# Performance work log

Measured on AMD Instinct MI355X. Metric: run time of the kernel, lower is better.

## Reference

```python
import jax, jax.numpy as jnp
import numpy as np

B, S, H, NH = 1, 4096, 768, 12
D = H // NH  # per-head dim = 64


def setup_inputs() -> dict:
    key = jax.random.key(0)
    ks = jax.random.split(key, 10)
    p = 0.02  # param scale
    return {
        "x": jax.random.normal(ks[0], (B, S, H), jnp.float32),
        "Wq": jax.random.normal(ks[1], (H, H), jnp.float32) * p,
        "bq": jax.random.normal(ks[2], (H,), jnp.float32) * p,
        "Wk": jax.random.normal(ks[3], (H, H), jnp.float32) * p,
        "bk": jax.random.normal(ks[4], (H,), jnp.float32) * p,
        "Wv": jax.random.normal(ks[5], (H, H), jnp.float32) * p,
        "bv": jax.random.normal(ks[6], (H,), jnp.float32) * p,
        "Wo": jax.random.normal(ks[7], (H, H), jnp.float32) * p,
        "bo": jax.random.normal(ks[8], (H,), jnp.float32) * p,
        "attn_mask": jax.random.randint(ks[9], (B, 1, 1, S), 0, 2).astype(bool),
    }


def _split_heads(t):
    # [B, S, H] -> [B, NH, S, D]
    return t.reshape(B, S, NH, D).transpose(0, 2, 1, 3)


def reference(x, Wq, bq, Wk, bk, Wv, bv, Wo, bo, attn_mask):
    q = _split_heads(x @ Wq.T + bq)
    k = _split_heads(x @ Wk.T + bk)
    v = _split_heads(x @ Wv.T + bv)
    scores = jnp.einsum('bhqd,bhkd->bhqk', q, k) / np.sqrt(D).astype(np.float32)
    scores = jnp.where(attn_mask, jnp.float32(-1e9), scores)
    attn = jax.nn.softmax(scores, axis=-1)
    ctx = jnp.einsum('bhqk,bhkd->bhqd', attn, v)
    ctx = ctx.transpose(0, 2, 1, 3).reshape(B, S, H)  # merge heads
    return ctx @ Wo.T + bo
```

## Files before the change

kernel.cpp:

```cpp
#include <hip/hip_runtime.h>
#include <stdint.h>

#define S_LEN 4096
#define HDIM  768
#define NHEAD 12
#define DHEAD 64

typedef _Float16 f16;
typedef __attribute__((ext_vector_type(8)))  _Float16 f16x8;
typedef __attribute__((ext_vector_type(4)))  _Float16 f16x4;
typedef __attribute__((ext_vector_type(4)))  float    f32x4;
typedef __attribute__((ext_vector_type(16))) float    f32x16;

typedef __attribute__((address_space(1))) void gv_t;
typedef __attribute__((address_space(3))) void lv_t;

__device__ __forceinline__ void async_copy16(const void* g, void* l) {
  __builtin_amdgcn_global_load_lds((gv_t*)g, (lv_t*)l, 16, 0, 0);
}

__device__ __forceinline__ float fast_exp2(float x) {
#if __has_builtin(__builtin_amdgcn_exp2f)
  return __builtin_amdgcn_exp2f(x);
#else
  return exp2f(x);
#endif
}

__device__ __forceinline__ int swz4(int row) { return (row ^ (row >> 2)) & 3; }

constexpr size_t OFF_META = 0;
constexpr size_t OFF_POS  = 256;
constexpr size_t OFF_XB   = 65536;
constexpr size_t SZ_XB    = (size_t)S_LEN * HDIM * 2;
constexpr size_t OFF_WQKV = OFF_XB + SZ_XB;
constexpr size_t SZ_WQKV  = (size_t)3 * HDIM * HDIM * 2;
constexpr size_t OFF_WO   = OFF_WQKV + SZ_WQKV;
constexpr size_t SZ_WO    = (size_t)HDIM * HDIM * 2;
constexpr size_t OFF_Q    = OFF_WO + SZ_WO;
constexpr size_t SZ_HD    = (size_t)NHEAD * S_LEN * DHEAD * 2;
constexpr size_t OFF_K    = OFF_Q + SZ_HD;
constexpr size_t OFF_VT   = OFF_K + SZ_HD;
constexpr size_t OFF_VR   = OFF_VT + SZ_HD;
constexpr size_t OFF_PO1  = OFF_VR + SZ_HD;

__global__ __launch_bounds__(256) void k_prep(const float* __restrict__ x,
                                              const float* __restrict__ wq,
                                              const float* __restrict__ wk,
                                              const float* __restrict__ wv,
                                              const float* __restrict__ wo,
                                              const int* __restrict__ mi,
                                              f16* __restrict__ dst,
                                              f16* __restrict__ Kc,
                                              int* __restrict__ pos,
                                              int* __restrict__ meta) {
  __shared__ int s_flag;
  __shared__ int s_cnt[256];
  const int b = blockIdx.x, tid = threadIdx.x;
  if (b < 5376) {
    int i = b * 256 + tid;
    const float* src; int off;
    if (i < 786432) { src = x; off = i; }
    else {
      int j = i - 786432;
      int w = j / 147456;
      off = j - w * 147456;
      src = (w == 0) ? wq : (w == 1) ? wk : (w == 2) ? wv : wo;
    }
    float4 v = ((const float4*)src)[off];
    f16x4 h;
    h[0] = (f16)v.x; h[1] = (f16)v.y; h[2] = (f16)v.z; h[3] = (f16)v.w;
    ((f16x4*)dst)[i] = h;
    return;
  }
  if (b < 6144) {
    int u = (b - 5376) * 512 + tid;
    f16x8 z = {};
    ((f16x8*)Kc)[u] = z;
    ((f16x8*)Kc)[u + 256] = z;
    return;
  }
  if (tid == 0) s_flag = 1;
  __syncthreads();
  int bad = 0;
  #pragma unroll
  for (int k = 0; k < 4; ++k) {
    int v = mi[k * 256 + tid];
    if (v != 0 && v != 1) bad = 1;
  }
  if (bad) atomicAnd(&s_flag, 0);
  __syncthreads();
  const int isInt = s_flag;
  const unsigned char* mu8 = (const unsigned char*)mi;
  int keep[16]; int cnt = 0;
  const int s0 = tid * 16;
  #pragma unroll
  for (int k = 0; k < 16; ++k) {
    int mval = isInt ? mi[s0 + k] : (int)mu8[s0 + k];
    keep[k] = (mval == 0) ? 1 : 0;
    cnt += keep[k];
  }
  s_cnt[tid] = cnt;
  __syncthreads();
  for (int off = 1; off < 256; off <<= 1) {
    int t = (tid >= off) ? s_cnt[tid - off] : 0;
    __syncthreads();
    s_cnt[tid] += t;
    __syncthreads();
  }
  int base = s_cnt[tid] - cnt;
  #pragma unroll
  for (int k = 0; k < 16; ++k) {
    pos[s0 + k] = keep[k] ? base : -1;
    base += keep[k];
  }
  if (tid == 255) meta[0] = s_cnt[255];
}

__global__ __launch_bounds__(256) void k_qkv(
    const f16* __restrict__ xb, const f16* __restrict__ wqkv,
    const float* __restrict__ bq, const float* __restrict__ bk, const float* __restrict__ bv,
    const int* __restrict__ pos,
    f16* __restrict__ Qh, f16* __restrict__ Kc, f16* __restrict__ Vrow) {
  __shared__ __attribute__((aligned(16))) f16 lA[128 * 32];
  __shared__ __attribute__((aligned(16))) f16 lB[128 * 32];
  const int tid = threadIdx.x;
  const int wid = tid >> 6, lane = tid & 63;
  const int quad = lane >> 4, l16 = lane & 15;
  const int wm = wid >> 1, wn = wid & 1;
  const int tn = blockIdx.x;
  const int m0 = blockIdx.y * 128;
  const int mat = tn / 6;
  const int nb = (tn % 6) * 128;
  const f16* wbase = wqkv + (size_t)mat * HDIM * HDIM;

  f32x4 acc[4][4] = {};

  for (int k0 = 0; k0 < HDIM; k0 += 32) {
    #pragma unroll
    for (int iss = 0; iss < 2; ++iss) {
      int c = iss * 256 + tid;
      int row = c >> 2, slot = c & 3;
      int gs = slot ^ swz4(row);
      async_copy16((const char*)(xb + (size_t)(m0 + row) * HDIM + k0) + gs * 16,
                   (char*)lA + (iss * 256 + wid * 64) * 16);
      async_copy16((const char*)(wbase + (size_t)(nb + row) * HDIM + k0) + gs * 16,
                   (char*)lB + (iss * 256 + wid * 64) * 16);
    }
    __syncthreads();
    f16x8 af[4], bf[4];
    #pragma unroll
    for (int mi = 0; mi < 4; ++mi) {
      int row = wm * 64 + mi * 16 + l16;
      af[mi] = *(const f16x8*)&lA[row * 32 + (quad ^ swz4(row)) * 8];
    }
    #pragma unroll
    for (int ni = 0; ni < 4; ++ni) {
      int row = wn * 64 + ni * 16 + l16;
      bf[ni] = *(const f16x8*)&lB[row * 32 + (quad ^ swz4(row)) * 8];
    }
    #pragma unroll
    for (int mi = 0; mi < 4; ++mi)
      #pragma unroll
      for (int ni = 0; ni < 4; ++ni)
        acc[mi][ni] = __builtin_amdgcn_mfma_f32_16x16x32_f16(af[mi], bf[ni], acc[mi][ni], 0, 0, 0);
    __syncthreads();
  }

  const float* bias = (mat == 0) ? bq : (mat == 1) ? bk : bv;
  const float qscale = 0.125f * 1.44269504088896341f;
  f16* kvdst = (mat == 1) ? Kc : Vrow;
  #pragma unroll
  for (int mi = 0; mi < 4; ++mi) {
    int srow = m0 + wm * 64 + mi * 16 + quad * 4;
    #pragma unroll
    for (int ni = 0; ni < 4; ++ni) {
      int n = nb + wn * 64 + ni * 16 + l16;
      int head = n >> 6, d = n & 63;
      float b = bias[n];
      #pragma unroll
      for (int r = 0; r < 4; ++r) {
        int s = srow + r;
        float val = acc[mi][ni][r] + b;
        if (mat == 0) {
          Qh[((size_t)head * S_LEN + s) * DHEAD + d] = (f16)(val * qscale);
        } else {
          int p = pos[s];
          if (p >= 0)
            kvdst[((size_t)head * S_LEN + p) * DHEAD + d] = (f16)val;
        }
      }
    }
  }
}

__global__ __launch_bounds__(256) void k_vt(const int* __restrict__ meta,
                                            const f16* __restrict__ Vrow,
                                            f16* __restrict__ Vtc) {
  const int kc = meta[0];
  const int kcp = (kc + 63) & ~63;
  const int p0 = blockIdx.x * 64;
  const int h = blockIdx.y;
  if (p0 >= kcp) return;
  __shared__ __attribute__((aligned(16))) f16 lT[64 * 80];
  const int tid = threadIdx.x;
  for (int u = tid; u < 512; u += 256) {
    int d8 = u >> 6, p = u & 63;
    f16x8 v = {};
    if (p0 + p < kc) v = *(const f16x8*)&Vrow[((size_t)h * S_LEN + p0 + p) * DHEAD + d8 * 8];
    #pragma unroll
    for (int j = 0; j < 8; ++j) lT[(d8 * 8 + j) * 80 + p] = v[j];
  }
  __syncthreads();
  for (int w = tid; w < 512; w += 256) {
    int d = w >> 3, p8 = w & 7;
    f16x8 o = *(const f16x8*)&lT[d * 80 + p8 * 8];
    *(f16x8*)&Vtc[((size_t)h * DHEAD + d) * S_LEN + p0 + p8 * 8] = o;
  }
}

__global__ __launch_bounds__(256) void k_attn(
    const f16* __restrict__ Qh, const f16* __restrict__ Kc, const f16* __restrict__ Vtc,
    const int* __restrict__ meta, f16* __restrict__ PO0, f16* __restrict__ PO1,
    float* __restrict__ PL) {
  __shared__ __attribute__((aligned(16))) f16 lK[64 * 64];
  __shared__ __attribute__((aligned(16))) f16 lV[64 * 64];
  __shared__ __attribute__((aligned(16))) f16 lP[4][32 * 64];
  const int tid = threadIdx.x;
  const int wid = tid >> 6, lane = tid & 63;
  const int hf = lane >> 5, q = lane & 31, r7 = q & 7;
  const int head = blockIdx.y;
  const int q0 = blockIdx.x * 128 + wid * 32;
  const int split = blockIdx.z;
  const int kc = meta[0];
  const int nkt = (kc + 63) >> 6;
  const int th = nkt >> 1;
  const int t0 = split ? th : 0;
  const int t1 = split ? nkt : th;
  const float npadf = split ? (float)(nkt * 64 - kc) : 0.f;

  const f16* Qp = Qh + ((size_t)head * S_LEN + q0 + q) * DHEAD;
  f16x8 qf[4];
  #pragma unroll
  for (int t = 0; t < 4; ++t) qf[t] = *(const f16x8*)(Qp + t * 16 + hf * 8);

  f32x16 accO0 = {}, accO1 = {};
  float lsum = 0.f;

  const char* kbase = (const char*)(Kc + (size_t)head * S_LEN * DHEAD);
  const char* vbase = (const char*)(Vtc + (size_t)head * DHEAD * S_LEN);
  f16* pw = &lP[wid][0];

  for (int it = t0; it < t1; ++it) {
    const int j0 = it * 64;
    #pragma unroll
    for (int iss = 0; iss < 2; ++iss) {
      int c = iss * 256 + tid;
      int row = c >> 3, slot = c & 7;
      int gs = slot ^ (row & 7);
      async_copy16(kbase + (size_t)(j0 + row) * 128 + gs * 16,
                   (char*)lK + (iss * 256 + wid * 64) * 16);
      async_copy16(vbase + (size_t)row * (S_LEN * 2) + (size_t)j0 * 2 + gs * 16,
                   (char*)lV + (iss * 256 + wid * 64) * 16);
    }
    __syncthreads();

    f32x16 sA = {}, sB = {};
    #pragma unroll
    for (int t = 0; t < 4; ++t) {
      int so = ((2 * t + hf) ^ r7) * 8;
      f16x8 a0 = *(const f16x8*)&lK[q * 64 + so];
      f16x8 a1 = *(const f16x8*)&lK[(32 + q) * 64 + so];
      sA = __builtin_amdgcn_mfma_f32_32x32x16_f16(a0, qf[t], sA, 0, 0, 0);
      sB = __builtin_amdgcn_mfma_f32_32x32x16_f16(a1, qf[t], sB, 0, 0, 0);
    }

    #pragma unroll
    for (int i = 0; i < 16; ++i) { sA[i] = fast_exp2(sA[i]); lsum += sA[i]; }
    #pragma unroll
    for (int i = 0; i < 16; ++i) { sB[i] = fast_exp2(sB[i]); lsum += sB[i]; }

    #pragma unroll
    for (int g = 0; g < 4; ++g) {
      f16x4 w0, w1;
      #pragma unroll
      for (int r = 0; r < 4; ++r) { w0[r] = (f16)sA[4 * g + r]; w1[r] = (f16)sB[4 * g + r]; }
      *(f16x4*)&pw[q * 64 + (g ^ r7) * 8 + hf * 4]       = w0;
      *(f16x4*)&pw[q * 64 + ((4 + g) ^ r7) * 8 + hf * 4] = w1;
    }

    #pragma unroll
    for (int t = 0; t < 4; ++t) {
      int so = ((2 * t + hf) ^ r7) * 8;
      f16x8 pf = *(const f16x8*)&pw[q * 64 + so];
      f16x8 v0 = *(const f16x8*)&lV[q * 64 + so];
      f16x8 v1 = *(const f16x8*)&lV[(32 + q) * 64 + so];
      accO0 = __builtin_amdgcn_mfma_f32_32x32x16_f16(pf, v0, accO0, 0, 0, 0);
      accO1 = __builtin_amdgcn_mfma_f32_32x32x16_f16(pf, v1, accO1, 0, 0, 0);
    }
    __syncthreads();
  }

  lsum += __shfl_xor(lsum, 32, 64);
  lsum -= npadf;
  if (hf == 0)
    PL[((size_t)split * NHEAD + head) * S_LEN + q0 + q] = lsum;

  f16* PO = split ? PO1 : PO0;
  #pragma unroll
  for (int reg = 0; reg < 16; ++reg) {
    int s = q0 + (reg & 3) + 8 * (reg >> 2) + 4 * hf;
    PO[((size_t)head * S_LEN + s) * DHEAD + q]      = (f16)accO0[reg];
    PO[((size_t)head * S_LEN + s) * DHEAD + 32 + q] = (f16)accO1[reg];
  }
}

__global__ __launch_bounds__(256) void k_comb(const f16* __restrict__ PO0,
                                              const f16* __restrict__ PO1,
                                              const float* __restrict__ PL,
                                              f16* __restrict__ ctx) {
  int u = blockIdx.x * 256 + threadIdx.x;
  int s = u / 96;
  int c = u - s * 96;
  int h = c >> 3, db = (c & 7) * 8;
  size_t i0 = ((size_t)h * S_LEN + s) * DHEAD + db;
  f16x8 o0 = *(const f16x8*)(PO0 + i0);
  f16x8 o1 = *(const f16x8*)(PO1 + i0);
  float l = PL[(size_t)h * S_LEN + s] + PL[(size_t)(NHEAD + h) * S_LEN + s];
  float inv = 1.0f / l;
  f16x8 o;
  #pragma unroll
  for (int i = 0; i < 8; ++i) o[i] = (f16)(((float)o0[i] + (float)o1[i]) * inv);
  *(f16x8*)(ctx + (size_t)s * HDIM + h * DHEAD + db) = o;
}

__global__ __launch_bounds__(256) void k_out(
    const f16* __restrict__ ctx, const f16* __restrict__ wo,
    const float* __restrict__ bo, float* __restrict__ out) {
  __shared__ __attribute__((aligned(16))) f16 lA[128 * 32];
  __shared__ __attribute__((aligned(16))) f16 lB[128 * 32];
  const int tid = threadIdx.x;
  const int wid = tid >> 6, lane = tid & 63;
  const int quad = lane >> 4, l16 = lane & 15;
  const int wm = wid >> 1, wn = wid & 1;
  const int nb = blockIdx.x * 128;
  const int m0 = blockIdx.y * 128;

  f32x4 acc[4][4] = {};

  for (int k0 = 0; k0 < HDIM; k0 += 32) {
    #pragma unroll
    for (int iss = 0; iss < 2; ++iss) {
      int c = iss * 256 + tid;
      int row = c >> 2, slot = c & 3;
      int gs = slot ^ swz4(row);
      async_copy16((const char*)(ctx + (size_t)(m0 + row) * HDIM + k0) + gs * 16,
                   (char*)lA + (iss * 256 + wid * 64) * 16);
      async_copy16((const char*)(wo + (size_t)(nb + row) * HDIM + k0) + gs * 16,
                   (char*)lB + (iss * 256 + wid * 64) * 16);
    }
    __syncthreads();
    f16x8 af[4], bf[4];
    #pragma unroll
    for (int mi = 0; mi < 4; ++mi) {
      int row = wm * 64 + mi * 16 + l16;
      af[mi] = *(const f16x8*)&lA[row * 32 + (quad ^ swz4(row)) * 8];
    }
    #pragma unroll
    for (int ni = 0; ni < 4; ++ni) {
      int row = wn * 64 + ni * 16 + l16;
      bf[ni] = *(const f16x8*)&lB[row * 32 + (quad ^ swz4(row)) * 8];
    }
    #pragma unroll
    for (int mi = 0; mi < 4; ++mi)
      #pragma unroll
      for (int ni = 0; ni < 4; ++ni)
        acc[mi][ni] = __builtin_amdgcn_mfma_f32_16x16x32_f16(af[mi], bf[ni], acc[mi][ni], 0, 0, 0);
    __syncthreads();
  }

  #pragma unroll
  for (int mi = 0; mi < 4; ++mi) {
    int srow = m0 + wm * 64 + mi * 16 + quad * 4;
    #pragma unroll
    for (int ni = 0; ni < 4; ++ni) {
      int n = nb + wn * 64 + ni * 16 + l16;
      float b = bo[n];
      #pragma unroll
      for (int r = 0; r < 4; ++r)
        out[(size_t)(srow + r) * HDIM + n] = acc[mi][ni][r] + b;
    }
  }
}

extern "C" void kernel_launch(void* const* d_in, const int* in_sizes, int n_in,
                              void* d_out, int out_size, void* d_ws, size_t ws_size,
                              hipStream_t stream) {
  const float* x  = (const float*)d_in[0];
  const float* Wq = (const float*)d_in[1];
  const float* bq = (const float*)d_in[2];
  const float* Wk = (const float*)d_in[3];
  const float* bk = (const float*)d_in[4];
  const float* Wv = (const float*)d_in[5];
  const float* bv = (const float*)d_in[6];
  const float* Wo = (const float*)d_in[7];
  const float* bo = (const float*)d_in[8];
  const int*   mask = (const int*)d_in[9];
  float* out = (float*)d_out;

  char* ws = (char*)d_ws;
  int* meta  = (int*)(ws + OFF_META);
  int* pos   = (int*)(ws + OFF_POS);
  f16* xb    = (f16*)(ws + OFF_XB);
  f16* wqkv  = (f16*)(ws + OFF_WQKV);
  f16* wob   = (f16*)(ws + OFF_WO);
  f16* Qh    = (f16*)(ws + OFF_Q);
  f16* Kc    = (f16*)(ws + OFF_K);
  f16* Vtc   = (f16*)(ws + OFF_VT);
  f16* Vrow  = (f16*)(ws + OFF_VR);
  f16* PO0   = (f16*)(ws + OFF_VR);
  f16* PO1   = (f16*)(ws + OFF_PO1);
  float* PL  = (float*)(ws + OFF_WQKV);
  f16* ctx   = (f16*)(ws + OFF_XB);

  k_prep<<<dim3(6145), 256, 0, stream>>>(x, Wq, Wk, Wv, Wo, mask, xb, Kc, pos, meta);
  k_qkv<<<dim3(18, 32), 256, 0, stream>>>(xb, wqkv, bq, bk, bv, pos, Qh, Kc, Vrow);
  k_vt<<<dim3(64, NHEAD), 256, 0, stream>>>(meta, Vrow, Vtc);
  k_attn<<<dim3(32, NHEAD, 2), 256, 0, stream>>>(Qh, Kc, Vtc, meta, PO0, PO1, PL);
  k_comb<<<dim3((S_LEN * 96) / 256), 256, 0, stream>>>(PO0, PO1, PL, ctx);
  k_out<<<dim3(6, 32), 256, 0, stream>>>(ctx, wob, bo, out);
}
```

Baseline: 192.4 us.

## Restructure attention kernel: 64-query warps, in-register P, intra-block key split

Each wavefront now handles 64 queries instead of 32, and the four warps split into two query groups times two key-tile streams. Each key stream owns its own K/V LDS buffer, loaded by separate warps. The exp'd scores are fed straight from registers into the PV MFMA, which removes the per-warp P round trip through LDS. The two key-stream partial outputs are merged through LDS at the end, and launch bounds request 3 blocks per CU. The V transpose store also now reads its LDS tile in 4-element pieces. The aim is more K/V reuse per LDS load and fewer LDS writes, at the cost of more accumulator registers and a final reduction step.

```diff
diff --git a/kernel.cpp b/kernel.cpp
--- a/kernel.cpp
+++ b/kernel.cpp
@@ -214,104 +214,154 @@
   __syncthreads();
   for (int w = tid; w < 512; w += 256) {
     int d = w >> 3, p8 = w & 7;
-    f16x8 o = *(const f16x8*)&lT[d * 80 + p8 * 8];
+    int base16 = (p8 >> 1) * 16, half = p8 & 1;
+    f16x4 lo = *(const f16x4*)&lT[d * 80 + base16 + half * 4];
+    f16x4 hi = *(const f16x4*)&lT[d * 80 + base16 + 8 + half * 4];
+    f16x8 o;
+    o[0] = lo[0]; o[1] = lo[1]; o[2] = lo[2]; o[3] = lo[3];
+    o[4] = hi[0]; o[5] = hi[1]; o[6] = hi[2]; o[7] = hi[3];
     *(f16x8*)&Vtc[((size_t)h * DHEAD + d) * S_LEN + p0 + p8 * 8] = o;
   }
 }
 
-__global__ __launch_bounds__(256) void k_attn(
+__global__ __launch_bounds__(256, 3) void k_attn(
     const f16* __restrict__ Qh, const f16* __restrict__ Kc, const f16* __restrict__ Vtc,
     const int* __restrict__ meta, f16* __restrict__ PO0, f16* __restrict__ PO1,
     float* __restrict__ PL) {
-  __shared__ __attribute__((aligned(16))) f16 lK[64 * 64];
-  __shared__ __attribute__((aligned(16))) f16 lV[64 * 64];
-  __shared__ __attribute__((aligned(16))) f16 lP[4][32 * 64];
+  __shared__ __attribute__((aligned(16))) f16 lbuf[2][2][64 * 64];
+  __shared__ float lcomb[2][64];
   const int tid = threadIdx.x;
   const int wid = tid >> 6, lane = tid & 63;
-  const int hf = lane >> 5, q = lane & 31, r7 = q & 7;
+  const int hf = lane >> 5, l31 = lane & 31;
+  const int qg = wid & 1, ks = wid >> 1;
   const int head = blockIdx.y;
-  const int q0 = blockIdx.x * 128 + wid * 32;
   const int split = blockIdx.z;
+  const int qbase = blockIdx.x * 128 + qg * 64;
   const int kc = meta[0];
   const int nkt = (kc + 63) >> 6;
   const int th = nkt >> 1;
   const int t0 = split ? th : 0;
   const int t1 = split ? nkt : th;
-  const float npadf = split ? (float)(nkt * 64 - kc) : 0.f;
-
-  const f16* Qp = Qh + ((size_t)head * S_LEN + q0 + q) * DHEAD;
-  f16x8 qf[4];
-  #pragma unroll
-  for (int t = 0; t < 4; ++t) qf[t] = *(const f16x8*)(Qp + t * 16 + hf * 8);
-
-  f32x16 accO0 = {}, accO1 = {};
-  float lsum = 0.f;
+  const int nloop = (t1 - t0 + 1) >> 1;
+
+  f16x8 qf[2][4];
+  #pragma unroll
+  for (int qh = 0; qh < 2; ++qh) {
+    const f16* Qp = Qh + ((size_t)head * S_LEN + qbase + qh * 32 + l31) * DHEAD;
+    #pragma unroll
+    for (int dc = 0; dc < 4; ++dc)
+      qf[qh][dc] = *(const f16x8*)(Qp + dc * 16 + hf * 8);
+  }
+
+  f32x16 accO[2][2] = {};
+  float lsum[2] = {0.f, 0.f};
 
   const char* kbase = (const char*)(Kc + (size_t)head * S_LEN * DHEAD);
   const char* vbase = (const char*)(Vtc + (size_t)head * DHEAD * S_LEN);
-  f16* pw = &lP[wid][0];
-
-  for (int it = t0; it < t1; ++it) {
-    const int j0 = it * 64;
-    #pragma unroll
-    for (int iss = 0; iss < 2; ++iss) {
-      int c = iss * 256 + tid;
-      int row = c >> 3, slot = c & 7;
-      int gs = slot ^ (row & 7);
-      async_copy16(kbase + (size_t)(j0 + row) * 128 + gs * 16,
-                   (char*)lK + (iss * 256 + wid * 64) * 16);
-      async_copy16(vbase + (size_t)row * (S_LEN * 2) + (size_t)j0 * 2 + gs * 16,
-                   (char*)lV + (iss * 256 + wid * 64) * 16);
-    }
-    __syncthreads();
-
-    f32x16 sA = {}, sB = {};
-    #pragma unroll
-    for (int t = 0; t < 4; ++t) {
-      int so = ((2 * t + hf) ^ r7) * 8;
-      f16x8 a0 = *(const f16x8*)&lK[q * 64 + so];
-      f16x8 a1 = *(const f16x8*)&lK[(32 + q) * 64 + so];
-      sA = __builtin_amdgcn_mfma_f32_32x32x16_f16(a0, qf[t], sA, 0, 0, 0);
-      sB = __builtin_amdgcn_mfma_f32_32x32x16_f16(a1, qf[t], sB, 0, 0, 0);
-    }
-
-    #pragma unroll
-    for (int i = 0; i < 16; ++i) { sA[i] = fast_exp2(sA[i]); lsum += sA[i]; }
-    #pragma unroll
-    for (int i = 0; i < 16; ++i) { sB[i] = fast_exp2(sB[i]); lsum += sB[i]; }
-
-    #pragma unroll
-    for (int g = 0; g < 4; ++g) {
-      f16x4 w0, w1;
-      #pragma unroll
-      for (int r = 0; r < 4; ++r) { w0[r] = (f16)sA[4 * g + r]; w1[r] = (f16)sB[4 * g + r]; }
-      *(f16x4*)&pw[q * 64 + (g ^ r7) * 8 + hf * 4]       = w0;
-      *(f16x4*)&pw[q * 64 + ((4 + g) ^ r7) * 8 + hf * 4] = w1;
-    }
-
-    #pragma unroll
-    for (int t = 0; t < 4; ++t) {
-      int so = ((2 * t + hf) ^ r7) * 8;
-      f16x8 pf = *(const f16x8*)&pw[q * 64 + so];
-      f16x8 v0 = *(const f16x8*)&lV[q * 64 + so];
-      f16x8 v1 = *(const f16x8*)&lV[(32 + q) * 64 + so];
-      accO0 = __builtin_amdgcn_mfma_f32_32x32x16_f16(pf, v0, accO0, 0, 0, 0);
-      accO1 = __builtin_amdgcn_mfma_f32_32x32x16_f16(pf, v1, accO1, 0, 0, 0);
-    }
-    __syncthreads();
-  }
-
-  lsum += __shfl_xor(lsum, 32, 64);
-  lsum -= npadf;
-  if (hf == 0)
-    PL[((size_t)split * NHEAD + head) * S_LEN + q0 + q] = lsum;
-
-  f16* PO = split ? PO1 : PO0;
-  #pragma unroll
-  for (int reg = 0; reg < 16; ++reg) {
-    int s = q0 + (reg & 3) + 8 * (reg >> 2) + 4 * hf;
-    PO[((size_t)head * S_LEN + s) * DHEAD + q]      = (f16)accO0[reg];
-    PO[((size_t)head * S_LEN + s) * DHEAD + 32 + q] = (f16)accO1[reg];
+  f16* myK = &lbuf[ks][0][0];
+  f16* myV = &lbuf[ks][1][0];
+  const int srow = lane >> 3, sslot = lane & 7;
+
+  for (int i = 0; i < nloop; ++i) {
+    const int t = t0 + 2 * i + ks;
+    const bool active = t < t1;
+    if (active) {
+      const int j0 = t * 64;
+      if (qg == 0) {
+        #pragma unroll
+        for (int r = 0; r < 8; ++r) {
+          int row = r * 8 + srow;
+          int gs = sslot ^ (row & 7);
+          async_copy16(kbase + (size_t)(j0 + row) * 128 + gs * 16, (char*)myK + r * 1024);
+        }
+      } else {
+        #pragma unroll
+        for (int r = 0; r < 8; ++r) {
+          int d = r * 8 + srow;
+          int gs = sslot ^ (d & 7);
+          async_copy16(vbase + (size_t)d * (S_LEN * 2) + (size_t)j0 * 2 + gs * 16,
+                       (char*)myV + r * 1024);
+        }
+      }
+    }
+    __syncthreads();
+    if (active) {
+      #pragma unroll
+      for (int mh = 0; mh < 2; ++mh) {
+        f16x8 af[4];
+        const int arow = mh * 32 + l31;
+        #pragma unroll
+        for (int dc = 0; dc < 4; ++dc) {
+          int c = dc * 2 + hf;
+          af[dc] = *(const f16x8*)&myK[arow * 64 + ((c ^ (arow & 7)) * 8)];
+        }
+        #pragma unroll
+        for (int qh = 0; qh < 2; ++qh) {
+          f32x16 s = {};
+          #pragma unroll
+          for (int dc = 0; dc < 4; ++dc)
+            s = __builtin_amdgcn_mfma_f32_32x32x16_f16(af[dc], qf[qh][dc], s, 0, 0, 0);
+          float ls = 0.f;
+          #pragma unroll
+          for (int u = 0; u < 16; ++u) { s[u] = fast_exp2(s[u]); ls += s[u]; }
+          lsum[qh] += ls;
+          #pragma unroll
+          for (int cc = 0; cc < 2; ++cc) {
+            f16x8 pf;
+            #pragma unroll
+            for (int u = 0; u < 8; ++u) pf[u] = (f16)s[8 * cc + u];
+            const int kt = mh * 2 + cc;
+            #pragma unroll
+            for (int dh = 0; dh < 2; ++dh) {
+              int vrow = dh * 32 + l31;
+              int c = kt * 2 + hf;
+              f16x8 vf = *(const f16x8*)&myV[vrow * 64 + ((c ^ (vrow & 7)) * 8)];
+              accO[qh][dh] = __builtin_amdgcn_mfma_f32_32x32x16_f16(pf, vf, accO[qh][dh], 0, 0, 0);
+            }
+          }
+        }
+      }
+    }
+    __syncthreads();
+  }
+
+  lsum[0] += __shfl_xor(lsum[0], 32);
+  lsum[1] += __shfl_xor(lsum[1], 32);
+  const float npadf = (float)(nkt * 64 - kc);
+  if (split == 1 && (((nkt - 1 - t0) & 1) == ks)) { lsum[0] -= npadf; lsum[1] -= npadf; }
+
+  float* ocomb = (float*)&lbuf[0][0][0];
+  if (ks == 1) {
+    #pragma unroll
+    for (int qh = 0; qh < 2; ++qh) {
+      #pragma unroll
+      for (int dh = 0; dh < 2; ++dh)
+        #pragma unroll
+        for (int reg = 0; reg < 16; ++reg) {
+          int row = qh * 32 + (reg & 3) + 8 * (reg >> 2) + 4 * hf;
+          ocomb[qg * 4096 + row * 64 + dh * 32 + l31] = accO[qh][dh][reg];
+        }
+      if (hf == 0) lcomb[qg][qh * 32 + l31] = lsum[qh];
+    }
+  }
+  __syncthreads();
+  if (ks == 0) {
+    f16* PO = split ? PO1 : PO0;
+    #pragma unroll
+    for (int qh = 0; qh < 2; ++qh) {
+      #pragma unroll
+      for (int dh = 0; dh < 2; ++dh)
+        #pragma unroll
+        for (int reg = 0; reg < 16; ++reg) {
+          int row = qh * 32 + (reg & 3) + 8 * (reg >> 2) + 4 * hf;
+          float v = accO[qh][dh][reg] + ocomb[qg * 4096 + row * 64 + dh * 32 + l31];
+          int sidx = qbase + row;
+          PO[((size_t)head * S_LEN + sidx) * DHEAD + dh * 32 + l31] = (f16)v;
+        }
+      if (hf == 0)
+        PL[((size_t)split * NHEAD + head) * S_LEN + qbase + qh * 32 + l31] =
+            lsum[qh] + lcomb[qg][qh * 32 + l31];
+    }
   }
 }
 
```

Measured after the change: 256.2 us. +33.2%, slower.

## Keep softmax probabilities in registers by permuting V columns to match MFMA layout

Applied to the files above, without the earlier changes.

The attention kernel no longer writes exp(scores) to per-wave LDS and reads them back as the A operand. Each 32-key score tile is converted to f16 in registers and fed straight into the PV MFMA. To keep that correct, the V transpose kernel interleaves groups of four keys so that V's key order matches the accumulator's register layout. The change also drops the lP shared buffer and adds an occupancy hint of 3 blocks per CU. It saves LDS traffic and capacity in the inner loop, at the cost of a tighter coupling between the V storage order and the MFMA output layout.

```diff
diff --git a/kernel.cpp b/kernel.cpp
--- a/kernel.cpp
+++ b/kernel.cpp
@@ -214,45 +214,47 @@
   __syncthreads();
   for (int w = tid; w < 512; w += 256) {
     int d = w >> 3, p8 = w & 7;
-    f16x8 o = *(const f16x8*)&lT[d * 80 + p8 * 8];
+    int base16 = (p8 >> 1) * 16, half = p8 & 1;
+    f16x4 lo = *(const f16x4*)&lT[d * 80 + base16 + half * 4];
+    f16x4 hi = *(const f16x4*)&lT[d * 80 + base16 + 8 + half * 4];
+    f16x8 o;
+    o[0] = lo[0]; o[1] = lo[1]; o[2] = lo[2]; o[3] = lo[3];
+    o[4] = hi[0]; o[5] = hi[1]; o[6] = hi[2]; o[7] = hi[3];
     *(f16x8*)&Vtc[((size_t)h * DHEAD + d) * S_LEN + p0 + p8 * 8] = o;
   }
 }
 
-__global__ __launch_bounds__(256) void k_attn(
+__global__ __launch_bounds__(256, 3) void k_attn(
     const f16* __restrict__ Qh, const f16* __restrict__ Kc, const f16* __restrict__ Vtc,
     const int* __restrict__ meta, f16* __restrict__ PO0, f16* __restrict__ PO1,
     float* __restrict__ PL) {
   __shared__ __attribute__((aligned(16))) f16 lK[64 * 64];
   __shared__ __attribute__((aligned(16))) f16 lV[64 * 64];
-  __shared__ __attribute__((aligned(16))) f16 lP[4][32 * 64];
   const int tid = threadIdx.x;
   const int wid = tid >> 6, lane = tid & 63;
-  const int hf = lane >> 5, q = lane & 31, r7 = q & 7;
+  const int hf = lane >> 5, l31 = lane & 31, r7 = l31 & 7;
   const int head = blockIdx.y;
+  const int split = blockIdx.z;
   const int q0 = blockIdx.x * 128 + wid * 32;
-  const int split = blockIdx.z;
   const int kc = meta[0];
   const int nkt = (kc + 63) >> 6;
   const int th = nkt >> 1;
   const int t0 = split ? th : 0;
   const int t1 = split ? nkt : th;
-  const float npadf = split ? (float)(nkt * 64 - kc) : 0.f;
-
-  const f16* Qp = Qh + ((size_t)head * S_LEN + q0 + q) * DHEAD;
+
+  const f16* Qp = Qh + ((size_t)head * S_LEN + q0 + l31) * DHEAD;
   f16x8 qf[4];
   #pragma unroll
-  for (int t = 0; t < 4; ++t) qf[t] = *(const f16x8*)(Qp + t * 16 + hf * 8);
-
-  f32x16 accO0 = {}, accO1 = {};
+  for (int dc = 0; dc < 4; ++dc) qf[dc] = *(const f16x8*)(Qp + dc * 16 + hf * 8);
+
+  f32x16 accO[2] = {};
   float lsum = 0.f;
 
   const char* kbase = (const char*)(Kc + (size_t)head * S_LEN * DHEAD);
   const char* vbase = (const char*)(Vtc + (size_t)head * DHEAD * S_LEN);
-  f16* pw = &lP[wid][0];
-
-  for (int it = t0; it < t1; ++it) {
-    const int j0 = it * 64;
+
+  for (int t = t0; t < t1; ++t) {
+    const int j0 = t * 64;
     #pragma unroll
     for (int iss = 0; iss < 2; ++iss) {
       int c = iss * 256 + tid;
@@ -265,54 +267,49 @@
     }
     __syncthreads();
 
-    f32x16 sA = {}, sB = {};
-    #pragma unroll
-    for (int t = 0; t < 4; ++t) {
-      int so = ((2 * t + hf) ^ r7) * 8;
-      f16x8 a0 = *(const f16x8*)&lK[q * 64 + so];
-      f16x8 a1 = *(const f16x8*)&lK[(32 + q) * 64 + so];
-      sA = __builtin_amdgcn_mfma_f32_32x32x16_f16(a0, qf[t], sA, 0, 0, 0);
-      sB = __builtin_amdgcn_mfma_f32_32x32x16_f16(a1, qf[t], sB, 0, 0, 0);
-    }
-
-    #pragma unroll
-    for (int i = 0; i < 16; ++i) { sA[i] = fast_exp2(sA[i]); lsum += sA[i]; }
-    #pragma unroll
-    for (int i = 0; i < 16; ++i) { sB[i] = fast_exp2(sB[i]); lsum += sB[i]; }
-
-    #pragma unroll
-    for (int g = 0; g < 4; ++g) {
-      f16x4 w0, w1;
-      #pragma unroll
-      for (int r = 0; r < 4; ++r) { w0[r] = (f16)sA[4 * g + r]; w1[r] = (f16)sB[4 * g + r]; }
-      *(f16x4*)&pw[q * 64 + (g ^ r7) * 8 + hf * 4]       = w0;
-      *(f16x4*)&pw[q * 64 + ((4 + g) ^ r7) * 8 + hf * 4] = w1;
-    }
-
-    #pragma unroll
-    for (int t = 0; t < 4; ++t) {
-      int so = ((2 * t + hf) ^ r7) * 8;
-      f16x8 pf = *(const f16x8*)&pw[q * 64 + so];
-      f16x8 v0 = *(const f16x8*)&lV[q * 64 + so];
-      f16x8 v1 = *(const f16x8*)&lV[(32 + q) * 64 + so];
-      accO0 = __builtin_amdgcn_mfma_f32_32x32x16_f16(pf, v0, accO0, 0, 0, 0);
-      accO1 = __builtin_amdgcn_mfma_f32_32x32x16_f16(pf, v1, accO1, 0, 0, 0);
-    }
-    __syncthreads();
-  }
-
-  lsum += __shfl_xor(lsum, 32, 64);
-  lsum -= npadf;
+    #pragma unroll
+    for (int mh = 0; mh < 2; ++mh) {
+      f16x8 af[4];
+      const int arow = mh * 32 + l31;
+      #pragma unroll
+      for (int dc = 0; dc < 4; ++dc)
+        af[dc] = *(const f16x8*)&lK[arow * 64 + ((((dc << 1) | hf) ^ r7) * 8)];
+      f32x16 s = {};
+      #pragma unroll
+      for (int dc = 0; dc < 4; ++dc)
+        s = __builtin_amdgcn_mfma_f32_32x32x16_f16(af[dc], qf[dc], s, 0, 0, 0);
+      #pragma unroll
+      for (int u = 0; u < 16; ++u) { s[u] = fast_exp2(s[u]); lsum += s[u]; }
+      #pragma unroll
+      for (int cc = 0; cc < 2; ++cc) {
+        f16x8 pf;
+        #pragma unroll
+        for (int u = 0; u < 8; ++u) pf[u] = (f16)s[8 * cc + u];
+        const int c2 = mh * 2 + cc;
+        #pragma unroll
+        for (int dh = 0; dh < 2; ++dh) {
+          const int vrow = dh * 32 + l31;
+          f16x8 vf = *(const f16x8*)&lV[vrow * 64 + ((((c2 << 1) | hf) ^ r7) * 8)];
+          accO[dh] = __builtin_amdgcn_mfma_f32_32x32x16_f16(pf, vf, accO[dh], 0, 0, 0);
+        }
+      }
+    }
+    __syncthreads();
+  }
+
+  lsum += __shfl_xor(lsum, 32);
+  if (split == 1) lsum -= (float)(nkt * 64 - kc);
   if (hf == 0)
-    PL[((size_t)split * NHEAD + head) * S_LEN + q0 + q] = lsum;
+    PL[((size_t)split * NHEAD + head) * S_LEN + q0 + l31] = lsum;
 
   f16* PO = split ? PO1 : PO0;
   #pragma unroll
-  for (int reg = 0; reg < 16; ++reg) {
-    int s = q0 + (reg & 3) + 8 * (reg >> 2) + 4 * hf;
-    PO[((size_t)head * S_LEN + s) * DHEAD + q]      = (f16)accO0[reg];
-    PO[((size_t)head * S_LEN + s) * DHEAD + 32 + q] = (f16)accO1[reg];
-  }
+  for (int dh = 0; dh < 2; ++dh)
+    #pragma unroll
+    for (int reg = 0; reg < 16; ++reg) {
+      int row = (reg & 3) + 8 * (reg >> 2) + 4 * hf;
+      PO[((size_t)head * S_LEN + q0 + row) * DHEAD + dh * 32 + l31] = (f16)accO[dh][reg];
+    }
 }
 
 __global__ __launch_bounds__(256) void k_comb(const f16* __restrict__ PO0,
```

Measured after the change: 186.7 us. -2.9%, faster.
